# Optimization experiments

Hardware: AMD Instinct MI355X
Metric: run time of the kernel (lower is better)

Reference implementation:

```python
import jax, jax.numpy as jnp
import numpy as np

T_STEPS, N, STATE, HID, ACT, C = 32, 64, 64, 128, 32, 96


def setup_inputs() -> dict:
    key = jax.random.key(0)
    ks = jax.random.split(key, 16)
    s = 0.05
    inp = {
        'x': jax.random.normal(ks[0], (T_STEPS, N, STATE), jnp.float32),
        'a': jax.random.normal(ks[1], (T_STEPS, N, ACT), jnp.float32),
        # GRU layer 0 (input state_dim) and layer 1 (input hidden_dim)
        'wih0': jax.random.normal(ks[2], (3 * HID, STATE), jnp.float32) * s,
        'whh0': jax.random.normal(ks[3], (3 * HID, HID), jnp.float32) * s,
        'bih0': jax.random.normal(ks[4], (3 * HID,), jnp.float32) * s,
        'bhh0': jax.random.normal(ks[5], (3 * HID,), jnp.float32) * s,
        'wih1': jax.random.normal(ks[6], (3 * HID, HID), jnp.float32) * s,
        'whh1': jax.random.normal(ks[7], (3 * HID, HID), jnp.float32) * s,
        'bih1': jax.random.normal(ks[8], (3 * HID,), jnp.float32) * s,
        'bhh1': jax.random.normal(ks[9], (3 * HID,), jnp.float32) * s,
        'w1': jax.random.normal(ks[10], (HID, HID + ACT), jnp.float32) * s,
        'b1': jax.random.normal(ks[11], (HID,), jnp.float32) * s,
        'w2': jax.random.normal(ks[12], (1, 2 * HID), jnp.float32) * s,
        'b2': jax.random.normal(ks[13], (1,), jnp.float32) * s,
        'Tm': jax.random.normal(ks[14], (HID, HID, C), jnp.float32),  # init.normal(T,0,1)
    }
    return inp


def _gru_cell(x_t, h, wih, whh, bih, bhh):
    gi = x_t @ wih.T + bih            # (N, 3H)
    gh = h @ whh.T + bhh
    i_r, i_z, i_n = jnp.split(gi, 3, axis=-1)
    h_r, h_z, h_n = jnp.split(gh, 3, axis=-1)
    r = jax.nn.sigmoid(i_r + h_r)
    z = jax.nn.sigmoid(i_z + h_z)
    n = jnp.tanh(i_n + r * h_n)
    return (1.0 - z) * n + z * h


def reference(x, a, wih0, whh0, bih0, bhh0, wih1, whh1, bih1, bhh1, w1, b1, w2, b2, Tm):
    def step(h, x_t):
        h0 = _gru_cell(x_t, h[0], wih0, whh0, bih0, bhh0)
        h1 = _gru_cell(h0, h[1], wih1, whh1, bih1, bhh1)
        return jnp.stack([h0, h1]), h1

    h_init = jnp.zeros((2, N, HID), x.dtype)
    _, p = jax.lax.scan(step, h_init, x)              # (T, N, H)

    fc1 = jax.nn.relu(jnp.concatenate([p, a], -1) @ w1.T + b1)  # (T, N, H)

    Tflat = Tm.reshape(HID, HID * C)

    def batch_discrim(xt):  # xt: (N, H)
        M = (xt @ Tflat).reshape(N, HID, C)           # (N, B, C)
        # pairwise L1 over C: (N, N, B)
        norm = jnp.abs(M[:, None] - M[None, :]).sum(-1)
        o_b = (jnp.exp(-norm).sum(0) - 1.0) / (N - 1)  # (N, B)
        return jnp.concatenate([xt, o_b], 1)          # (N, 2H)

    fc2 = jax.lax.map(batch_discrim, fc1)             # (T, N, 2H)
    prob = jax.nn.sigmoid(fc2 @ w2.T + b2)            # (T, N, 1)
    return prob
```

## Files before the change

kernel.cpp:

```cpp
#include <hip/hip_runtime.h>
#include <hip/hip_fp16.h>
#include <cstdint>

#define T_STEPS 32
#define NB 64
#define STATE 64
#define HID 128
#define ACT 32
#define CDIM 96
#define G3 (3*HID)

typedef __attribute__((ext_vector_type(8))) short short8;
typedef __attribute__((ext_vector_type(4))) float f32x4;
typedef _Float16 h2v __attribute__((ext_vector_type(2)));

__device__ __forceinline__ unsigned short f2bf(float f){
  unsigned int u = __builtin_bit_cast(unsigned int, f);
  u = u + 0x7FFFu + ((u >> 16) & 1u);
  return (unsigned short)(u >> 16);
}
__device__ __forceinline__ float bf2f(unsigned short u){
  unsigned int v = ((unsigned int)u) << 16; return __builtin_bit_cast(float, v);
}
__device__ __forceinline__ unsigned int packh2(float f0, float f1){
  return (unsigned int)__half_as_ushort(__float2half_rn(f0)) |
         ((unsigned int)__half_as_ushort(__float2half_rn(f1)) << 16);
}
__device__ __forceinline__ float sigmoidf_(float x){ return 1.0f/(1.0f + __expf(-x)); }
__device__ __forceinline__ float tanhf_(float x){ float e = __expf(2.0f*x); return (e-1.0f)/(e+1.0f); }

__device__ __forceinline__ float dot2f(float acc, unsigned int a, unsigned int b){
  h2v av = __builtin_bit_cast(h2v, a);
  h2v bv = __builtin_bit_cast(h2v, b);
  return __builtin_amdgcn_fdot2(av, bv, acc, false);
}
__device__ __forceinline__ float l1d(float acc, unsigned int ua, unsigned int ub){
  __half2 a = __builtin_bit_cast(__half2, ua);
  __half2 b = __builtin_bit_cast(__half2, ub);
  __half2 d = __habs2(__hsub2(a, b));
  h2v dv = __builtin_bit_cast(h2v, d);
  h2v ones; ones[0] = (_Float16)1.0f; ones[1] = (_Float16)1.0f;
  return __builtin_amdgcn_fdot2(dv, ones, acc, false);
}
__device__ __forceinline__ float l1d4(float acc, uint4 a, uint4 b){
  acc = l1d(acc, a.x, b.x); acc = l1d(acc, a.y, b.y);
  acc = l1d(acc, a.z, b.z); acc = l1d(acc, a.w, b.w);
  return acc;
}

__global__ void k_prep(const float* __restrict__ Tm, unsigned short* __restrict__ tmh,
                       const float* __restrict__ whh0, const float* __restrict__ whh1,
                       const float* __restrict__ w1, const float* __restrict__ wih0,
                       const float* __restrict__ wih1, const float* __restrict__ a,
                       unsigned int* __restrict__ whh0p, unsigned int* __restrict__ whh1p,
                       unsigned short* __restrict__ w1f, unsigned int* __restrict__ wih0p,
                       unsigned int* __restrict__ wih1p, unsigned short* __restrict__ h1af){
  int tid = threadIdx.x;
  int bx = blockIdx.x;
  if (bx < 128){
    int b = bx;
    for (int e = tid; e < HID*CDIM; e += 256){
      int chunk = e / 768;
      int r1 = e - chunk*768;
      int c = r1 >> 3, h = r1 & 7;
      int k = chunk*8 + h;
      tmh[b*(HID*CDIM) + e] = f2bf(Tm[k*(HID*CDIM) + b*CDIM + c]);
    }
  } else if (bx < 132){
    for (int e = (bx-128)*256 + tid; e < 24576; e += 1024){
      int k2 = e / 384, r = e - k2*384;
      whh0p[e] = packh2(whh0[r*128 + 2*k2], whh0[r*128 + 2*k2 + 1]);
      whh1p[e] = packh2(whh1[r*128 + 2*k2], whh1[r*128 + 2*k2 + 1]);
    }
  } else if (bx < 136){
    for (int e = (bx-132)*256 + tid; e < 20480; e += 1024){
      int kc = e >> 10, rem = e & 1023;
      int col = rem >> 3, j = rem & 7;
      w1f[e] = f2bf(w1[col*160 + kc*8 + j]);
    }
  } else if (bx < 138){
    for (int e = (bx-136)*256 + tid; e < 12288; e += 512){
      int k2 = e / 384, r = e - k2*384;
      wih0p[e] = packh2(wih0[r*64 + 2*k2], wih0[r*64 + 2*k2 + 1]);
    }
  } else if (bx < 142){
    for (int e = (bx-138)*256 + tid; e < 24576; e += 1024){
      int k2 = e / 384, r = e - k2*384;
      wih1p[e] = packh2(wih1[r*128 + 2*k2], wih1[r*128 + 2*k2 + 1]);
    }
  } else {
    for (int e = (bx-142)*256 + tid; e < 65536; e += 3072){
      int t = e >> 11, rem = e & 2047;
      int n = rem >> 5, c = rem & 31;
      int pos = t*10240 + (n>>4)*2560 + (16 + (c>>3))*128 + (n&15)*8 + (c&7);
      h1af[pos] = f2bf(a[t*(NB*ACT) + n*ACT + c]);
    }
  }
}

__global__ __launch_bounds__(768, 3) void k_rec0(const float* __restrict__ x,
                                                 const unsigned int* __restrict__ wihp,
                                                 const unsigned int* __restrict__ whhp,
                                                 const float* __restrict__ bih, const float* __restrict__ bhh,
                                                 unsigned short* __restrict__ h0g){
  __shared__ __align__(16) unsigned int xall[1024];
  __shared__ __align__(16) unsigned int hl[64];
  __shared__ float A0[G3];
  __shared__ float GI[2][G3];
  int n = blockIdx.x, tid = threadIdx.x;
  int r = tid >> 1, kh = tid & 1;
  unsigned int wh[32], wi[16];
  #pragma unroll
  for (int i = 0; i < 32; i++) wh[i] = whhp[(kh*32 + i)*384 + r];
  #pragma unroll
  for (int i = 0; i < 16; i++) wi[i] = wihp[(kh*16 + i)*384 + r];
  float bh = (kh == 0) ? bhh[r] : 0.0f;
  float bi = (kh == 0) ? bih[r] : 0.0f;
  for (int e = tid; e < 1024; e += 768){
    int t_ = e >> 5, i = e & 31;
    const float* xp = x + t_*(NB*STATE) + n*STATE + 2*i;
    xall[e] = packh2(xp[0], xp[1]);
  }
  if (tid < 64) hl[tid] = 0u;
  float hprev = 0.0f;
  __syncthreads();
  const uint4* xl4 = (const uint4*)xall;
  const uint4* h4  = (const uint4*)hl;
  {
    float gi = bi;
    #pragma unroll
    for (int j = 0; j < 4; j++){
      uint4 xv = xl4[kh*4 + j];
      gi = dot2f(gi, wi[j*4 + 0], xv.x);
      gi = dot2f(gi, wi[j*4 + 1], xv.y);
      gi = dot2f(gi, wi[j*4 + 2], xv.z);
      gi = dot2f(gi, wi[j*4 + 3], xv.w);
    }
    gi += __shfl_xor(gi, 1);
    if (kh == 0) GI[0][r] = gi;
  }
  __syncthreads();
  for (int t = 0; t < T_STEPS; t++){
    float gh = bh, gin = bi;
    #pragma unroll
    for (int g = 0; g < 2; g++){
      uint4 hv[4];
      #pragma unroll
      for (int j = 0; j < 4; j++) hv[j] = h4[kh*8 + g*4 + j];
      #pragma unroll
      for (int j = 0; j < 4; j++){
        gh = dot2f(gh, wh[g*16 + j*4 + 0], hv[j].x);
        gh = dot2f(gh, wh[g*16 + j*4 + 1], hv[j].y);
        gh = dot2f(gh, wh[g*16 + j*4 + 2], hv[j].z);
        gh = dot2f(gh, wh[g*16 + j*4 + 3], hv[j].w);
      }
    }
    if (t + 1 < T_STEPS){
      #pragma unroll
      for (int j = 0; j < 4; j++){
        uint4 xv = xl4[(t+1)*8 + kh*4 + j];
        gin = dot2f(gin, wi[j*4 + 0], xv.x);
        gin = dot2f(gin, wi[j*4 + 1], xv.y);
        gin = dot2f(gin, wi[j*4 + 2], xv.z);
        gin = dot2f(gin, wi[j*4 + 3], xv.w);
      }
    }
    gh  += __shfl_xor(gh, 1);
    gin += __shfl_xor(gin, 1);
    if (kh == 0){
      A0[r] = gh;
      if (t + 1 < T_STEPS) GI[(t+1)&1][r] = gin;
    }
    __syncthreads();
    if (tid < HID){
      const float* gi = GI[t&1];
      float rg = sigmoidf_(gi[tid]       + A0[tid]);
      float z  = sigmoidf_(gi[tid+HID]   + A0[tid+HID]);
      float nn = tanhf_   (gi[tid+2*HID] + rg*A0[tid+2*HID]);
      float hn = (1.0f - z)*nn + z*hprev;
      hprev = hn;
      ((__half*)hl)[tid] = __float2half_rn(hn);
      h0g[n*4096 + t*128 + tid] = __half_as_ushort(__float2half_rn(hn));
    }
    __syncthreads();
  }
}

__global__ __launch_bounds__(768, 3) void k_rec1(const unsigned short* __restrict__ h0g,
                                                 const unsigned int* __restrict__ wihp,
                                                 const unsigned int* __restrict__ whhp,
                                                 const float* __restrict__ bih, const float* __restrict__ bhh,
                                                 unsigned short* __restrict__ h1af){
  __shared__ __align__(16) unsigned int h0all[2048];
  __shared__ __align__(16) unsigned int hl[64];
  __shared__ float A0[G3];
  __shared__ float GI[2][G3];
  int n = blockIdx.x, tid = threadIdx.x;
  int r = tid >> 1, kh = tid & 1;
  unsigned int wh[32], wi[32];
  #pragma unroll
  for (int i = 0; i < 32; i++) wh[i] = whhp[(kh*32 + i)*384 + r];
  #pragma unroll
  for (int i = 0; i < 32; i++) wi[i] = wihp[(kh*32 + i)*384 + r];
  float bh = (kh == 0) ? bhh[r] : 0.0f;
  float bi = (kh == 0) ? bih[r] : 0.0f;
  const unsigned int* h0u = (const unsigned int*)h0g;
  for (int e = tid; e < 2048; e += 768) h0all[e] = h0u[n*2048 + e];
  if (tid < 64) hl[tid] = 0u;
  float hprev = 0.0f;
  __syncthreads();
  const uint4* h0l4 = (const uint4*)h0all;
  const uint4* h4   = (const uint4*)hl;
  {
    float gi = bi;
    #pragma unroll
    for (int g = 0; g < 2; g++){
      #pragma unroll
      for (int j = 0; j < 4; j++){
        uint4 hv = h0l4[kh*8 + g*4 + j];
        gi = dot2f(gi, wi[g*16 + j*4 + 0], hv.x);
        gi = dot2f(gi, wi[g*16 + j*4 + 1], hv.y);
        gi = dot2f(gi, wi[g*16 + j*4 + 2], hv.z);
        gi = dot2f(gi, wi[g*16 + j*4 + 3], hv.w);
      }
    }
    gi += __shfl_xor(gi, 1);
    if (kh == 0) GI[0][r] = gi;
  }
  __syncthreads();
  for (int t = 0; t < T_STEPS; t++){
    float gh = bh, gin = bi;
    #pragma unroll
    for (int g = 0; g < 2; g++){
      uint4 hv[4];
      #pragma unroll
      for (int j = 0; j < 4; j++) hv[j] = h4[kh*8 + g*4 + j];
      #pragma unroll
      for (int j = 0; j < 4; j++){
        gh = dot2f(gh, wh[g*16 + j*4 + 0], hv[j].x);
        gh = dot2f(gh, wh[g*16 + j*4 + 1], hv[j].y);
        gh = dot2f(gh, wh[g*16 + j*4 + 2], hv[j].z);
        gh = dot2f(gh, wh[g*16 + j*4 + 3], hv[j].w);
      }
    }
    if (t + 1 < T_STEPS){
      #pragma unroll
      for (int g = 0; g < 2; g++){
        #pragma unroll
        for (int j = 0; j < 4; j++){
          uint4 hv = h0l4[(t+1)*16 + kh*8 + g*4 + j];
          gin = dot2f(gin, wi[g*16 + j*4 + 0], hv.x);
          gin = dot2f(gin, wi[g*16 + j*4 + 1], hv.y);
          gin = dot2f(gin, wi[g*16 + j*4 + 2], hv.z);
          gin = dot2f(gin, wi[g*16 + j*4 + 3], hv.w);
        }
      }
    }
    gh  += __shfl_xor(gh, 1);
    gin += __shfl_xor(gin, 1);
    if (kh == 0){
      A0[r] = gh;
      if (t + 1 < T_STEPS) GI[(t+1)&1][r] = gin;
    }
    __syncthreads();
    if (tid < HID){
      const float* gi = GI[t&1];
      float rg = sigmoidf_(gi[tid]       + A0[tid]);
      float z  = sigmoidf_(gi[tid+HID]   + A0[tid+HID]);
      float nn = tanhf_   (gi[tid+2*HID] + rg*A0[tid+2*HID]);
      float hn = (1.0f - z)*nn + z*hprev;
      hprev = hn;
      ((__half*)hl)[tid] = __float2half_rn(hn);
      h1af[t*10240 + (n>>4)*2560 + (tid>>3)*128 + (n&15)*8 + (tid&7)] = f2bf(hn);
    }
    __syncthreads();
  }
}

__global__ __launch_bounds__(256) void k_fc1(const unsigned short* __restrict__ h1af,
                                             const unsigned short* __restrict__ w1f,
                                             const float* __restrict__ b1,
                                             unsigned short* __restrict__ fc1h){
  __shared__ float b1s[128];
  int t = blockIdx.x, tid = threadIdx.x;
  int wave = tid >> 6, lane = tid & 63, m = lane & 15, quad = lane >> 4;
  if (tid < 128) b1s[tid] = b1[tid];
  const uint4* A4 = (const uint4*)(h1af + t*10240);
  const uint4* B4 = (const uint4*)w1f;
  f32x4 acc[8];
  #pragma unroll
  for (int i = 0; i < 8; i++) acc[i] = (f32x4)(0.0f);
  #pragma unroll
  for (int ks = 0; ks < 5; ks++){
    uint4 av = A4[wave*320 + (ks*4 + quad)*16 + m];
    short8 avs = __builtin_bit_cast(short8, av);
    #pragma unroll
    for (int nt = 0; nt < 8; nt++){
      uint4 bv = B4[(ks*4 + quad)*128 + nt*16 + m];
      acc[nt] = __builtin_amdgcn_mfma_f32_16x16x32_bf16(avs, __builtin_bit_cast(short8, bv), acc[nt], 0, 0, 0);
    }
  }
  __syncthreads();
  #pragma unroll
  for (int nt = 0; nt < 8; nt++){
    float bj = b1s[nt*16 + m];
    #pragma unroll
    for (int rr = 0; rr < 4; rr++){
      float v = fmaxf(acc[nt][rr] + bj, 0.0f);
      fc1h[t*8192 + wave*2048 + (nt*2 + (m>>3))*128 + (quad*4 + rr)*8 + (m&7)] = f2bf(v);
    }
  }
}

__global__ __launch_bounds__(256) void k_disc(const unsigned short* __restrict__ fc1h,
                                              const unsigned short* __restrict__ tmh,
                                              float* __restrict__ O){
  __shared__ __align__(16) __half Mh[2][64*104];
  __shared__ float ps[2][64*18];
  int b = blockIdx.x;
  int tid = threadIdx.x;
  int wave = tid >> 6, lane = tid & 63, m = lane & 15, quad = lane >> 4;
  int t0 = blockIdx.y*4;
  const uint4* Bg = (const uint4*)(tmh + b*(CDIM*HID));
  uint4 a4[4];
  #pragma unroll
  for (int kk = 0; kk < 4; kk++) a4[kk] = ((const uint4*)(fc1h + t0*8192))[wave*256 + (kk*4 + quad)*16 + m];
  #pragma unroll 1
  for (int tt = 0; tt < 4; tt++){
    int p = tt & 1;
    int t = t0 + tt;
    f32x4 acc[6];
    #pragma unroll
    for (int i = 0; i < 6; i++) acc[i] = (f32x4)(0.0f);
    #pragma unroll
    for (int kk = 0; kk < 4; kk++){
      short8 av = __builtin_bit_cast(short8, a4[kk]);
      #pragma unroll
      for (int nt = 0; nt < 6; nt++){
        uint4 b4 = Bg[(kk*4 + quad)*96 + nt*16 + m];
        acc[nt] = __builtin_amdgcn_mfma_f32_16x16x32_bf16(av, __builtin_bit_cast(short8, b4), acc[nt], 0, 0, 0);
      }
    }
    if (tt < 3){
      #pragma unroll
      for (int kk = 0; kk < 4; kk++) a4[kk] = ((const uint4*)(fc1h + (t+1)*8192))[wave*256 + (kk*4 + quad)*16 + m];
    }
    #pragma unroll
    for (int nt = 0; nt < 6; nt++){
      #pragma unroll
      for (int rr = 0; rr < 4; rr++){
        Mh[p][(rr*16 + wave*4 + quad)*104 + nt*16 + m] = __float2half(acc[nt][rr]);
      }
    }
    __syncthreads();
    if (tt > 0 && tid < NB){
      float s = 0.0f;
      #pragma unroll
      for (int k = 0; k < 16; k++) s += ps[1-p][tid*18 + k];
      O[((t-1)*HID + b)*NB + tid] = s*(1.0f/63.0f);
    }
    const uint4* M4 = (const uint4*)Mh[p];
    if (tid < 240){
      int chalf = tid & 1, tp = tid >> 1;
      int rnd = tp >> 3, slot = tp & 7;
      int ta, tb;
      if (slot == 0){ ta = 15; tb = rnd; }
      else {
        ta = rnd + slot;      if (ta >= 15) ta -= 15;
        tb = rnd + 15 - slot; if (tb >= 15) tb -= 15;
      }
      float facc[16];
      #pragma unroll
      for (int pp = 0; pp < 16; pp++) facc[pp] = 0.0f;
      auto doChunk = [&](int c){
        int ch = chalf*6 + c;
        uint4 av[4], bv[4];
        #pragma unroll
        for (int s = 0; s < 4; s++){
          av[s] = M4[(s*16 + ta)*13 + ch];
          bv[s] = M4[(s*16 + tb)*13 + ch];
        }
        #pragma unroll
        for (int i = 0; i < 4; i++)
          #pragma unroll
          for (int j = 0; j < 4; j++)
            facc[i*4+j] = l1d4(facc[i*4+j], av[i], bv[j]);
      };
      doChunk(0); doChunk(1);
      bool big1 = true;
      #pragma unroll
      for (int pp = 0; pp < 16; pp++) big1 = big1 && (facc[pp] > 14.0f);
      if (!big1){
        doChunk(2); doChunk(3);
        bool big2 = true;
        #pragma unroll
        for (int pp = 0; pp < 16; pp++) big2 = big2 && (facc[pp] > 14.0f);
        if (!big2){ doChunk(4); doChunk(5); }
      }
      float tot[16];
      #pragma unroll
      for (int pp = 0; pp < 16; pp++) tot[pp] = facc[pp] + __shfl_xor(facc[pp], 1);
      if (chalf == 0){
        #pragma unroll
        for (int i = 0; i < 4; i++){
          float s = 0.0f;
          #pragma unroll
          for (int j = 0; j < 4; j++) s += __expf(-tot[i*4+j]);
          ps[p][(ta*4 + i)*18 + tb] = s;
        }
      } else {
        #pragma unroll
        for (int j = 0; j < 4; j++){
          float s = 0.0f;
          #pragma unroll
          for (int i = 0; i < 4; i++) s += __expf(-tot[i*4+j]);
          ps[p][(tb*4 + j)*18 + ta] = s;
        }
      }
    } else {
      int ta = tid - 240;
      float f6[6];
      #pragma unroll
      for (int pp = 0; pp < 6; pp++) f6[pp] = 0.0f;
      auto doChunkS = [&](int ch){
        uint4 rv[4];
        #pragma unroll
        for (int s = 0; s < 4; s++) rv[s] = M4[(s*16 + ta)*13 + ch];
        f6[0] = l1d4(f6[0], rv[0], rv[1]);
        f6[1] = l1d4(f6[1], rv[0], rv[2]);
        f6[2] = l1d4(f6[2], rv[0], rv[3]);
        f6[3] = l1d4(f6[3], rv[1], rv[2]);
        f6[4] = l1d4(f6[4], rv[1], rv[3]);
        f6[5] = l1d4(f6[5], rv[2], rv[3]);
      };
      doChunkS(0); doChunkS(1); doChunkS(2);
      bool big1 = true;
      #pragma unroll
      for (int pp = 0; pp < 6; pp++) big1 = big1 && (f6[pp] > 14.0f);
      if (!big1){
        doChunkS(3); doChunkS(4); doChunkS(5);
        bool big2 = true;
        #pragma unroll
        for (int pp = 0; pp < 6; pp++) big2 = big2 && (f6[pp] > 14.0f);
        if (!big2){
          doChunkS(6); doChunkS(7); doChunkS(8);
          doChunkS(9); doChunkS(10); doChunkS(11);
        }
      }
      float e01 = __expf(-f6[0]), e02 = __expf(-f6[1]), e03 = __expf(-f6[2]);
      float e12 = __expf(-f6[3]), e13 = __expf(-f6[4]), e23 = __expf(-f6[5]);
      ps[p][(ta*4 + 0)*18 + ta] = e01 + e02 + e03;
      ps[p][(ta*4 + 1)*18 + ta] = e01 + e12 + e13;
      ps[p][(ta*4 + 2)*18 + ta] = e02 + e12 + e23;
      ps[p][(ta*4 + 3)*18 + ta] = e03 + e13 + e23;
    }
  }
  __syncthreads();
  if (tid < NB){
    float s = 0.0f;
    #pragma unroll
    for (int k = 0; k < 16; k++) s += ps[1][tid*18 + k];
    O[((t0+3)*HID + b)*NB + tid] = s*(1.0f/63.0f);
  }
}

__global__ __launch_bounds__(256) void k_final(const unsigned short* __restrict__ fc1h,
                                               const float* __restrict__ O,
                                               const float* __restrict__ w2, const float* __restrict__ b2,
                                               float* __restrict__ out){
  __shared__ float ol[NB*HID];
  __shared__ unsigned short fr[8192];
  __shared__ float wl[2*HID + 2];
  int t = blockIdx.x, tid = threadIdx.x;
  for (int i = tid; i < NB*HID; i += 256) ol[i] = O[t*NB*HID + i];
  const uint4* Fg = (const uint4*)(fc1h + t*8192);
  for (int i = tid; i < 1024; i += 256) ((uint4*)fr)[i] = Fg[i];
  if (tid < 2*HID) wl[tid] = w2[tid];
  if (tid == 0) wl[2*HID] = b2[0];
  __syncthreads();
  if (tid < NB){
    float acc = wl[2*HID];
    int base = (tid>>4)*2048 + (tid&15)*8;
    #pragma unroll 8
    for (int j = 0; j < HID; j++) acc += bf2f(fr[base + (j>>3)*128 + (j&7)])*wl[j];
    #pragma unroll 8
    for (int b = 0; b < HID; b++) acc += ol[b*NB + tid]*wl[HID + b];
    out[t*NB + tid] = sigmoidf_(acc);
  }
}

extern "C" void kernel_launch(void* const* d_in, const int* in_sizes, int n_in,
                              void* d_out, int out_size, void* d_ws, size_t ws_size,
                              hipStream_t stream){
  const float* x    = (const float*)d_in[0];
  const float* a    = (const float*)d_in[1];
  const float* wih0 = (const float*)d_in[2];
  const float* whh0 = (const float*)d_in[3];
  const float* bih0 = (const float*)d_in[4];
  const float* bhh0 = (const float*)d_in[5];
  const float* wih1 = (const float*)d_in[6];
  const float* whh1 = (const float*)d_in[7];
  const float* bih1 = (const float*)d_in[8];
  const float* bhh1 = (const float*)d_in[9];
  const float* w1   = (const float*)d_in[10];
  const float* b1   = (const float*)d_in[11];
  const float* w2   = (const float*)d_in[12];
  const float* b2   = (const float*)d_in[13];
  const float* Tm   = (const float*)d_in[14];
  float* ws = (float*)d_ws;
  float* Ows = ws;
  unsigned int* whh0p = (unsigned int*)(ws + 262144);
  unsigned int* whh1p = (unsigned int*)(ws + 286720);
  unsigned int* wih0p = (unsigned int*)(ws + 311296);
  unsigned int* wih1p = (unsigned int*)(ws + 323584);
  unsigned short* tmh  = (unsigned short*)(ws + 348160);
  unsigned short* fc1h = (unsigned short*)(ws + 1134592);
  unsigned short* h1af = (unsigned short*)(ws + 1265664);
  unsigned short* w1f  = (unsigned short*)(ws + 1429504);
  unsigned short* h0g  = (unsigned short*)(ws + 1439744);
  float* out = (float*)d_out;

  k_prep<<<dim3(154), dim3(256), 0, stream>>>(Tm, tmh, whh0, whh1, w1, wih0, wih1, a,
                                              whh0p, whh1p, w1f, wih0p, wih1p, h1af);
  k_rec0<<<dim3(NB), dim3(768), 0, stream>>>(x, wih0p, whh0p, bih0, bhh0, h0g);
  k_rec1<<<dim3(NB), dim3(768), 0, stream>>>(h0g, wih1p, whh1p, bih1, bhh1, h1af);
  k_fc1<<<dim3(T_STEPS), dim3(256), 0, stream>>>(h1af, w1f, b1, fc1h);
  k_disc<<<dim3(HID, T_STEPS/4), dim3(256), 0, stream>>>(fc1h, tmh, Ows);
  k_final<<<dim3(T_STEPS), dim3(256), 0, stream>>>(fc1h, Ows, w2, b2, out);
}
```

Baseline: 210.3 us.

## Restructure GRU recurrence to one thread per gate row, add finer early-exit checks

The GRU recurrence kernels now give each thread a full gate row (4 lanes per hidden unit, one idle) instead of splitting the K dimension across two threads. Gate pre-activations are passed between lanes with shuffles rather than shared memory, and the hidden state is double-buffered, which removes one block barrier per timestep. The prep kernel doubles the number of blocks used to transpose Tm. The discriminator's early-exit threshold is now checked after fewer chunks. The costs are more registers per thread (up to 128 weight words), a quarter of the lanes sitting idle, and more branch checks in the discriminator.

```diff
diff --git a/kernel.cpp b/kernel.cpp
--- a/kernel.cpp
+++ b/kernel.cpp
@@ -57,39 +57,39 @@
                        unsigned int* __restrict__ wih1p, unsigned short* __restrict__ h1af){
   int tid = threadIdx.x;
   int bx = blockIdx.x;
-  if (bx < 128){
-    int b = bx;
-    for (int e = tid; e < HID*CDIM; e += 256){
+  if (bx < 256){
+    int b = bx >> 1, half = bx & 1;
+    for (int e = half*6144 + tid; e < (half+1)*6144; e += 256){
       int chunk = e / 768;
       int r1 = e - chunk*768;
       int c = r1 >> 3, h = r1 & 7;
       int k = chunk*8 + h;
       tmh[b*(HID*CDIM) + e] = f2bf(Tm[k*(HID*CDIM) + b*CDIM + c]);
     }
-  } else if (bx < 132){
-    for (int e = (bx-128)*256 + tid; e < 24576; e += 1024){
+  } else if (bx < 260){
+    for (int e = (bx-256)*256 + tid; e < 24576; e += 1024){
       int k2 = e / 384, r = e - k2*384;
       whh0p[e] = packh2(whh0[r*128 + 2*k2], whh0[r*128 + 2*k2 + 1]);
       whh1p[e] = packh2(whh1[r*128 + 2*k2], whh1[r*128 + 2*k2 + 1]);
     }
-  } else if (bx < 136){
-    for (int e = (bx-132)*256 + tid; e < 20480; e += 1024){
+  } else if (bx < 264){
+    for (int e = (bx-260)*256 + tid; e < 20480; e += 1024){
       int kc = e >> 10, rem = e & 1023;
       int col = rem >> 3, j = rem & 7;
       w1f[e] = f2bf(w1[col*160 + kc*8 + j]);
     }
-  } else if (bx < 138){
-    for (int e = (bx-136)*256 + tid; e < 12288; e += 512){
+  } else if (bx < 266){
+    for (int e = (bx-264)*256 + tid; e < 12288; e += 512){
       int k2 = e / 384, r = e - k2*384;
       wih0p[e] = packh2(wih0[r*64 + 2*k2], wih0[r*64 + 2*k2 + 1]);
     }
-  } else if (bx < 142){
-    for (int e = (bx-138)*256 + tid; e < 24576; e += 1024){
+  } else if (bx < 270){
+    for (int e = (bx-266)*256 + tid; e < 24576; e += 1024){
       int k2 = e / 384, r = e - k2*384;
       wih1p[e] = packh2(wih1[r*128 + 2*k2], wih1[r*128 + 2*k2 + 1]);
     }
   } else {
-    for (int e = (bx-142)*256 + tid; e < 65536; e += 3072){
+    for (int e = (bx-270)*256 + tid; e < 65536; e += 3072){
       int t = e >> 11, rem = e & 2047;
       int n = rem >> 5, c = rem & 31;
       int pos = t*10240 + (n>>4)*2560 + (16 + (c>>3))*128 + (n&15)*8 + (c&7);
@@ -98,181 +98,167 @@
   }
 }
 
-__global__ __launch_bounds__(768, 3) void k_rec0(const float* __restrict__ x,
+__global__ __launch_bounds__(512, 2) void k_rec0(const float* __restrict__ x,
                                                  const unsigned int* __restrict__ wihp,
                                                  const unsigned int* __restrict__ whhp,
                                                  const float* __restrict__ bih, const float* __restrict__ bhh,
                                                  unsigned short* __restrict__ h0g){
   __shared__ __align__(16) unsigned int xall[1024];
-  __shared__ __align__(16) unsigned int hl[64];
-  __shared__ float A0[G3];
-  __shared__ float GI[2][G3];
+  __shared__ __align__(16) unsigned int hb[2][64];
   int n = blockIdx.x, tid = threadIdx.x;
-  int r = tid >> 1, kh = tid & 1;
-  unsigned int wh[32], wi[16];
-  #pragma unroll
-  for (int i = 0; i < 32; i++) wh[i] = whhp[(kh*32 + i)*384 + r];
-  #pragma unroll
-  for (int i = 0; i < 16; i++) wi[i] = wihp[(kh*16 + i)*384 + r];
-  float bh = (kh == 0) ? bhh[r] : 0.0f;
-  float bi = (kh == 0) ? bih[r] : 0.0f;
-  for (int e = tid; e < 1024; e += 768){
-    int t_ = e >> 5, i = e & 31;
-    const float* xp = x + t_*(NB*STATE) + n*STATE + 2*i;
+  int i = tid >> 2, c = tid & 3;
+  bool act = (c < 3);
+  int row = c*128 + i;
+  unsigned int wh[64], wi[32];
+  if (act){
+    #pragma unroll
+    for (int k = 0; k < 64; k++) wh[k] = whhp[k*384 + row];
+    #pragma unroll
+    for (int k = 0; k < 32; k++) wi[k] = wihp[k*384 + row];
+  }
+  float bh = act ? bhh[row] : 0.0f;
+  float bi = act ? bih[row] : 0.0f;
+  for (int e = tid; e < 1024; e += 512){
+    int t_ = e >> 5, j = e & 31;
+    const float* xp = x + t_*(NB*STATE) + n*STATE + 2*j;
     xall[e] = packh2(xp[0], xp[1]);
   }
-  if (tid < 64) hl[tid] = 0u;
+  if (tid < 64) hb[0][tid] = 0u;
   float hprev = 0.0f;
   __syncthreads();
   const uint4* xl4 = (const uint4*)xall;
-  const uint4* h4  = (const uint4*)hl;
+  float gic;
   {
-    float gi = bi;
-    #pragma unroll
-    for (int j = 0; j < 4; j++){
-      uint4 xv = xl4[kh*4 + j];
-      gi = dot2f(gi, wi[j*4 + 0], xv.x);
-      gi = dot2f(gi, wi[j*4 + 1], xv.y);
-      gi = dot2f(gi, wi[j*4 + 2], xv.z);
-      gi = dot2f(gi, wi[j*4 + 3], xv.w);
-    }
-    gi += __shfl_xor(gi, 1);
-    if (kh == 0) GI[0][r] = gi;
-  }
-  __syncthreads();
+    float a0 = bi, a1 = 0.f, a2 = 0.f, a3 = 0.f;
+    #pragma unroll
+    for (int j = 0; j < 8; j++){
+      uint4 xv = xl4[j];
+      a0 = dot2f(a0, wi[j*4+0], xv.x);
+      a1 = dot2f(a1, wi[j*4+1], xv.y);
+      a2 = dot2f(a2, wi[j*4+2], xv.z);
+      a3 = dot2f(a3, wi[j*4+3], xv.w);
+    }
+    gic = (a0+a1)+(a2+a3);
+  }
   for (int t = 0; t < T_STEPS; t++){
-    float gh = bh, gin = bi;
-    #pragma unroll
-    for (int g = 0; g < 2; g++){
-      uint4 hv[4];
-      #pragma unroll
-      for (int j = 0; j < 4; j++) hv[j] = h4[kh*8 + g*4 + j];
-      #pragma unroll
-      for (int j = 0; j < 4; j++){
-        gh = dot2f(gh, wh[g*16 + j*4 + 0], hv[j].x);
-        gh = dot2f(gh, wh[g*16 + j*4 + 1], hv[j].y);
-        gh = dot2f(gh, wh[g*16 + j*4 + 2], hv[j].z);
-        gh = dot2f(gh, wh[g*16 + j*4 + 3], hv[j].w);
-      }
-    }
+    const uint4* hb4 = (const uint4*)hb[t & 1];
+    float b0 = bh, b1 = 0.f, b2 = 0.f, b3 = 0.f;
+    #pragma unroll
+    for (int j = 0; j < 16; j++){
+      uint4 hv = hb4[j];
+      b0 = dot2f(b0, wh[j*4+0], hv.x);
+      b1 = dot2f(b1, wh[j*4+1], hv.y);
+      b2 = dot2f(b2, wh[j*4+2], hv.z);
+      b3 = dot2f(b3, wh[j*4+3], hv.w);
+    }
+    float gh = (b0+b1)+(b2+b3);
+    float gin = 0.0f;
     if (t + 1 < T_STEPS){
-      #pragma unroll
-      for (int j = 0; j < 4; j++){
-        uint4 xv = xl4[(t+1)*8 + kh*4 + j];
-        gin = dot2f(gin, wi[j*4 + 0], xv.x);
-        gin = dot2f(gin, wi[j*4 + 1], xv.y);
-        gin = dot2f(gin, wi[j*4 + 2], xv.z);
-        gin = dot2f(gin, wi[j*4 + 3], xv.w);
-      }
-    }
-    gh  += __shfl_xor(gh, 1);
-    gin += __shfl_xor(gin, 1);
-    if (kh == 0){
-      A0[r] = gh;
-      if (t + 1 < T_STEPS) GI[(t+1)&1][r] = gin;
-    }
-    __syncthreads();
-    if (tid < HID){
-      const float* gi = GI[t&1];
-      float rg = sigmoidf_(gi[tid]       + A0[tid]);
-      float z  = sigmoidf_(gi[tid+HID]   + A0[tid+HID]);
-      float nn = tanhf_   (gi[tid+2*HID] + rg*A0[tid+2*HID]);
+      float a0 = bi, a1 = 0.f, a2 = 0.f, a3 = 0.f;
+      #pragma unroll
+      for (int j = 0; j < 8; j++){
+        uint4 xv = xl4[(t+1)*8 + j];
+        a0 = dot2f(a0, wi[j*4+0], xv.x);
+        a1 = dot2f(a1, wi[j*4+1], xv.y);
+        a2 = dot2f(a2, wi[j*4+2], xv.z);
+        a3 = dot2f(a3, wi[j*4+3], xv.w);
+      }
+      gin = (a0+a1)+(a2+a3);
+    }
+    float zp  = __shfl_down(gic + gh, 1);
+    float gnn = __shfl_down(gic, 2);
+    float ghn = __shfl_down(gh, 2);
+    if (c == 0){
+      float rg = sigmoidf_(gic + gh);
+      float z  = sigmoidf_(zp);
+      float nn = tanhf_(gnn + rg*ghn);
       float hn = (1.0f - z)*nn + z*hprev;
       hprev = hn;
-      ((__half*)hl)[tid] = __float2half_rn(hn);
-      h0g[n*4096 + t*128 + tid] = __half_as_ushort(__float2half_rn(hn));
-    }
+      ((__half*)hb[(t+1) & 1])[i] = __float2half_rn(hn);
+      h0g[n*4096 + t*128 + i] = __half_as_ushort(__float2half_rn(hn));
+    }
+    gic = gin;
     __syncthreads();
   }
 }
 
-__global__ __launch_bounds__(768, 3) void k_rec1(const unsigned short* __restrict__ h0g,
+__global__ __launch_bounds__(512, 2) void k_rec1(const unsigned short* __restrict__ h0g,
                                                  const unsigned int* __restrict__ wihp,
                                                  const unsigned int* __restrict__ whhp,
                                                  const float* __restrict__ bih, const float* __restrict__ bhh,
                                                  unsigned short* __restrict__ h1af){
   __shared__ __align__(16) unsigned int h0all[2048];
-  __shared__ __align__(16) unsigned int hl[64];
-  __shared__ float A0[G3];
-  __shared__ float GI[2][G3];
+  __shared__ __align__(16) unsigned int hb[2][64];
   int n = blockIdx.x, tid = threadIdx.x;
-  int r = tid >> 1, kh = tid & 1;
-  unsigned int wh[32], wi[32];
-  #pragma unroll
-  for (int i = 0; i < 32; i++) wh[i] = whhp[(kh*32 + i)*384 + r];
-  #pragma unroll
-  for (int i = 0; i < 32; i++) wi[i] = wihp[(kh*32 + i)*384 + r];
-  float bh = (kh == 0) ? bhh[r] : 0.0f;
-  float bi = (kh == 0) ? bih[r] : 0.0f;
+  int i = tid >> 2, c = tid & 3;
+  bool act = (c < 3);
+  int row = c*128 + i;
+  unsigned int wh[64], wi[64];
+  if (act){
+    #pragma unroll
+    for (int k = 0; k < 64; k++) wh[k] = whhp[k*384 + row];
+    #pragma unroll
+    for (int k = 0; k < 64; k++) wi[k] = wihp[k*384 + row];
+  }
+  float bh = act ? bhh[row] : 0.0f;
+  float bi = act ? bih[row] : 0.0f;
   const unsigned int* h0u = (const unsigned int*)h0g;
-  for (int e = tid; e < 2048; e += 768) h0all[e] = h0u[n*2048 + e];
-  if (tid < 64) hl[tid] = 0u;
+  for (int e = tid; e < 2048; e += 512) h0all[e] = h0u[n*2048 + e];
+  if (tid < 64) hb[0][tid] = 0u;
   float hprev = 0.0f;
   __syncthreads();
   const uint4* h0l4 = (const uint4*)h0all;
-  const uint4* h4   = (const uint4*)hl;
+  float gic;
   {
-    float gi = bi;
-    #pragma unroll
-    for (int g = 0; g < 2; g++){
-      #pragma unroll
-      for (int j = 0; j < 4; j++){
-        uint4 hv = h0l4[kh*8 + g*4 + j];
-        gi = dot2f(gi, wi[g*16 + j*4 + 0], hv.x);
-        gi = dot2f(gi, wi[g*16 + j*4 + 1], hv.y);
-        gi = dot2f(gi, wi[g*16 + j*4 + 2], hv.z);
-        gi = dot2f(gi, wi[g*16 + j*4 + 3], hv.w);
-      }
-    }
-    gi += __shfl_xor(gi, 1);
-    if (kh == 0) GI[0][r] = gi;
-  }
-  __syncthreads();
+    float a0 = bi, a1 = 0.f, a2 = 0.f, a3 = 0.f;
+    #pragma unroll
+    for (int j = 0; j < 16; j++){
+      uint4 hv = h0l4[j];
+      a0 = dot2f(a0, wi[j*4+0], hv.x);
+      a1 = dot2f(a1, wi[j*4+1], hv.y);
+      a2 = dot2f(a2, wi[j*4+2], hv.z);
+      a3 = dot2f(a3, wi[j*4+3], hv.w);
+    }
+    gic = (a0+a1)+(a2+a3);
+  }
   for (int t = 0; t < T_STEPS; t++){
-    float gh = bh, gin = bi;
-    #pragma unroll
-    for (int g = 0; g < 2; g++){
-      uint4 hv[4];
-      #pragma unroll
-      for (int j = 0; j < 4; j++) hv[j] = h4[kh*8 + g*4 + j];
-      #pragma unroll
-      for (int j = 0; j < 4; j++){
-        gh = dot2f(gh, wh[g*16 + j*4 + 0], hv[j].x);
-        gh = dot2f(gh, wh[g*16 + j*4 + 1], hv[j].y);
-        gh = dot2f(gh, wh[g*16 + j*4 + 2], hv[j].z);
-        gh = dot2f(gh, wh[g*16 + j*4 + 3], hv[j].w);
-      }
-    }
+    const uint4* hb4 = (const uint4*)hb[t & 1];
+    float b0 = bh, b1 = 0.f, b2 = 0.f, b3 = 0.f;
+    #pragma unroll
+    for (int j = 0; j < 16; j++){
+      uint4 hv = hb4[j];
+      b0 = dot2f(b0, wh[j*4+0], hv.x);
+      b1 = dot2f(b1, wh[j*4+1], hv.y);
+      b2 = dot2f(b2, wh[j*4+2], hv.z);
+      b3 = dot2f(b3, wh[j*4+3], hv.w);
+    }
+    float gh = (b0+b1)+(b2+b3);
+    float gin = 0.0f;
     if (t + 1 < T_STEPS){
-      #pragma unroll
-      for (int g = 0; g < 2; g++){
-        #pragma unroll
-        for (int j = 0; j < 4; j++){
-          uint4 hv = h0l4[(t+1)*16 + kh*8 + g*4 + j];
-          gin = dot2f(gin, wi[g*16 + j*4 + 0], hv.x);
-          gin = dot2f(gin, wi[g*16 + j*4 + 1], hv.y);
-          gin = dot2f(gin, wi[g*16 + j*4 + 2], hv.z);
-          gin = dot2f(gin, wi[g*16 + j*4 + 3], hv.w);
-        }
-      }
-    }
-    gh  += __shfl_xor(gh, 1);
-    gin += __shfl_xor(gin, 1);
-    if (kh == 0){
-      A0[r] = gh;
-      if (t + 1 < T_STEPS) GI[(t+1)&1][r] = gin;
-    }
-    __syncthreads();
-    if (tid < HID){
-      const float* gi = GI[t&1];
-      float rg = sigmoidf_(gi[tid]       + A0[tid]);
-      float z  = sigmoidf_(gi[tid+HID]   + A0[tid+HID]);
-      float nn = tanhf_   (gi[tid+2*HID] + rg*A0[tid+2*HID]);
+      float a0 = bi, a1 = 0.f, a2 = 0.f, a3 = 0.f;
+      #pragma unroll
+      for (int j = 0; j < 16; j++){
+        uint4 hv = h0l4[(t+1)*16 + j];
+        a0 = dot2f(a0, wi[j*4+0], hv.x);
+        a1 = dot2f(a1, wi[j*4+1], hv.y);
+        a2 = dot2f(a2, wi[j*4+2], hv.z);
+        a3 = dot2f(a3, wi[j*4+3], hv.w);
+      }
+      gin = (a0+a1)+(a2+a3);
+    }
+    float zp  = __shfl_down(gic + gh, 1);
+    float gnn = __shfl_down(gic, 2);
+    float ghn = __shfl_down(gh, 2);
+    if (c == 0){
+      float rg = sigmoidf_(gic + gh);
+      float z  = sigmoidf_(zp);
+      float nn = tanhf_(gnn + rg*ghn);
       float hn = (1.0f - z)*nn + z*hprev;
       hprev = hn;
-      ((__half*)hl)[tid] = __float2half_rn(hn);
-      h1af[t*10240 + (n>>4)*2560 + (tid>>3)*128 + (n&15)*8 + (tid&7)] = f2bf(hn);
-    }
+      ((__half*)hb[(t+1) & 1])[i] = __float2half_rn(hn);
+      h1af[t*10240 + (n>>4)*2560 + (i>>3)*128 + (n&15)*8 + (i&7)] = f2bf(hn);
+    }
+    gic = gin;
     __syncthreads();
   }
 }
@@ -386,16 +372,19 @@
           for (int j = 0; j < 4; j++)
             facc[i*4+j] = l1d4(facc[i*4+j], av[i], bv[j]);
       };
-      doChunk(0); doChunk(1);
-      bool big1 = true;
-      #pragma unroll
-      for (int pp = 0; pp < 16; pp++) big1 = big1 && (facc[pp] > 14.0f);
-      if (!big1){
-        doChunk(2); doChunk(3);
-        bool big2 = true;
-        #pragma unroll
-        for (int pp = 0; pp < 16; pp++) big2 = big2 && (facc[pp] > 14.0f);
-        if (!big2){ doChunk(4); doChunk(5); }
+      auto allBig = [&](){
+        bool big = true;
+        #pragma unroll
+        for (int pp = 0; pp < 16; pp++) big = big && (facc[pp] > 14.0f);
+        return big;
+      };
+      doChunk(0);
+      if (!allBig()){
+        doChunk(1);
+        if (!allBig()){
+          doChunk(2); doChunk(3);
+          if (!allBig()){ doChunk(4); doChunk(5); }
+        }
       }
       float tot[16];
       #pragma unroll
@@ -433,18 +422,18 @@
         f6[4] = l1d4(f6[4], rv[1], rv[3]);
         f6[5] = l1d4(f6[5], rv[2], rv[3]);
       };
-      doChunkS(0); doChunkS(1); doChunkS(2);
-      bool big1 = true;
-      #pragma unroll
-      for (int pp = 0; pp < 6; pp++) big1 = big1 && (f6[pp] > 14.0f);
-      if (!big1){
-        doChunkS(3); doChunkS(4); doChunkS(5);
-        bool big2 = true;
-        #pragma unroll
-        for (int pp = 0; pp < 6; pp++) big2 = big2 && (f6[pp] > 14.0f);
-        if (!big2){
-          doChunkS(6); doChunkS(7); doChunkS(8);
-          doChunkS(9); doChunkS(10); doChunkS(11);
+      auto allBigS = [&](){
+        bool big = true;
+        #pragma unroll
+        for (int pp = 0; pp < 6; pp++) big = big && (f6[pp] > 14.0f);
+        return big;
+      };
+      doChunkS(0); doChunkS(1);
+      if (!allBigS()){
+        doChunkS(2); doChunkS(3);
+        if (!allBigS()){
+          doChunkS(4); doChunkS(5); doChunkS(6); doChunkS(7);
+          doChunkS(8); doChunkS(9); doChunkS(10); doChunkS(11);
         }
       }
       float e01 = __expf(-f6[0]), e02 = __expf(-f6[1]), e03 = __expf(-f6[2]);
@@ -520,10 +509,10 @@
   unsigned short* h0g  = (unsigned short*)(ws + 1439744);
   float* out = (float*)d_out;
 
-  k_prep<<<dim3(154), dim3(256), 0, stream>>>(Tm, tmh, whh0, whh1, w1, wih0, wih1, a,
+  k_prep<<<dim3(282), dim3(256), 0, stream>>>(Tm, tmh, whh0, whh1, w1, wih0, wih1, a,
                                               whh0p, whh1p, w1f, wih0p, wih1p, h1af);
-  k_rec0<<<dim3(NB), dim3(768), 0, stream>>>(x, wih0p, whh0p, bih0, bhh0, h0g);
-  k_rec1<<<dim3(NB), dim3(768), 0, stream>>>(h0g, wih1p, whh1p, bih1, bhh1, h1af);
+  k_rec0<<<dim3(NB), dim3(512), 0, stream>>>(x, wih0p, whh0p, bih0, bhh0, h0g);
+  k_rec1<<<dim3(NB), dim3(512), 0, stream>>>(h0g, wih1p, whh1p, bih1, bhh1, h1af);
   k_fc1<<<dim3(T_STEPS), dim3(256), 0, stream>>>(h1af, w1f, b1, fc1h);
   k_disc<<<dim3(HID, T_STEPS/4), dim3(256), 0, stream>>>(fc1h, tmh, Ows);
   k_final<<<dim3(T_STEPS), dim3(256), 0, stream>>>(fc1h, Ows, w2, b2, out);
```

Measured after the change: 232.4 us. +10.5%, slower.
